# Kernel tuning notes

Measured on AMD Instinct MI355X. Metric: run time of the kernel, lower is better.

The kernel has to match this reference:

```python
import jax, jax.numpy as jnp
import numpy as np

D_MODEL = 1024
D_INNER = 2048   # expand * d_model
D_STATE = 16
D_CONV = 4
DT_RANK = 64     # ceil(d_model / 16)
BATCH = 4
SEQLEN = 2048


def _dw_causal_conv(x, w, b):
    # x: (B, d, L); w: (d, 1, K) depthwise; causal left pad K-1 -> output length L
    y = jax.lax.conv_general_dilated(
        x, w, window_strides=(1,), padding=[(D_CONV - 1, 0)],
        dimension_numbers=("NCH", "OIH", "NCH"), feature_group_count=x.shape[1])
    return y + b[None, :, None]


def _ssm_pass(x_conv, z, A_log, x_proj_w, dt_proj_w, dt_proj_b, D):
    # x_conv, z: (B, d, L)
    Bsz, d, L = x_conv.shape
    u = jax.nn.silu(x_conv)                                   # (B, d, L)
    x_dbl = jnp.einsum("bdl,rd->blr", u, x_proj_w)            # (B, L, dt_rank+2N)
    dt = x_dbl[..., :DT_RANK]
    Bm = x_dbl[..., DT_RANK:DT_RANK + D_STATE]                # (B, L, N)
    Cm = x_dbl[..., DT_RANK + D_STATE:]                       # (B, L, N)
    delta = jax.nn.softplus(jnp.einsum("blr,dr->bld", dt, dt_proj_w) + dt_proj_b)  # (B, L, d)
    A = -jnp.exp(A_log)                                       # (d, N)

    # time-major inputs for scan
    delta_t = jnp.transpose(delta, (1, 0, 2))                 # (L, B, d)
    u_t = jnp.transpose(u, (2, 0, 1))                         # (L, B, d)
    Bm_t = jnp.transpose(Bm, (1, 0, 2))                       # (L, B, N)
    Cm_t = jnp.transpose(Cm, (1, 0, 2))                       # (L, B, N)

    def step(h, inp):
        d_s, B_s, C_s, u_s = inp                              # (B,d) (B,N) (B,N) (B,d)
        dA = jnp.exp(d_s[:, :, None] * A)                     # (B, d, N)
        h = dA * h + (d_s * u_s)[:, :, None] * B_s[:, None, :]
        y = jnp.einsum("bdn,bn->bd", h, C_s)
        return h, y

    h0 = jnp.zeros((Bsz, d, D_STATE), dtype=u.dtype)
    _, ys = jax.lax.scan(step, h0, (delta_t, Bm_t, Cm_t, u_t))  # ys: (L, B, d)
    y = jnp.transpose(ys, (1, 2, 0)) + D[None, :, None] * u     # (B, d, L)
    return y * jax.nn.silu(z)


def setup_inputs() -> dict:
    key = jax.random.key(0)
    ks = jax.random.split(key, 16)
    s = 0.02
    hidden_states = jax.random.normal(ks[0], (BATCH, SEQLEN, D_MODEL), jnp.float32)
    in_proj_w = jax.random.normal(ks[1], (2 * D_INNER, D_MODEL), jnp.float32) * s
    conv_w_f = jax.random.normal(ks[2], (D_INNER, 1, D_CONV), jnp.float32) * 0.2
    conv_b_f = jax.random.normal(ks[3], (D_INNER,), jnp.float32) * 0.1
    conv_w_b = jax.random.normal(ks[4], (D_INNER, 1, D_CONV), jnp.float32) * 0.2
    conv_b_b = jax.random.normal(ks[5], (D_INNER,), jnp.float32) * 0.1
    x_proj_w_f = jax.random.normal(ks[6], (DT_RANK + 2 * D_STATE, D_INNER), jnp.float32) * s
    dt_proj_w_f = jax.random.uniform(ks[7], (D_INNER, DT_RANK), jnp.float32, -DT_RANK**-0.5, DT_RANK**-0.5)
    x_proj_w_b = jax.random.normal(ks[8], (DT_RANK + 2 * D_STATE, D_INNER), jnp.float32) * s
    dt_proj_w_b = jax.random.uniform(ks[9], (D_INNER, DT_RANK), jnp.float32, -DT_RANK**-0.5, DT_RANK**-0.5)
    # dt bias init: inverse-softplus of dt sampled log-uniform in [1e-3, 1e-1]
    dt = jnp.exp(jax.random.uniform(ks[10], (D_INNER,)) * (np.log(0.1) - np.log(0.001)) + np.log(0.001))
    dt = jnp.clip(dt, 1e-4, None)
    inv_dt = dt + jnp.log(-jnp.expm1(-dt))
    dt_proj_b_f = inv_dt
    dt_proj_b_b = inv_dt
    A_log = jnp.log(jnp.broadcast_to(jnp.arange(1, D_STATE + 1, dtype=jnp.float32), (D_INNER, D_STATE)))
    out_proj_w = jax.random.normal(ks[11], (D_MODEL, D_INNER), jnp.float32) * s
    return {
        "hidden_states": hidden_states, "in_proj_w": in_proj_w,
        "conv_w_f": conv_w_f, "conv_b_f": conv_b_f, "conv_w_b": conv_w_b, "conv_b_b": conv_b_b,
        "x_proj_w_f": x_proj_w_f, "dt_proj_w_f": dt_proj_w_f, "dt_proj_b_f": dt_proj_b_f,
        "x_proj_w_b": x_proj_w_b, "dt_proj_w_b": dt_proj_w_b, "dt_proj_b_b": dt_proj_b_b,
        "A_log_f": A_log, "A_log_b": A_log,
        "D_f": jnp.ones((D_INNER,), jnp.float32), "D_b": jnp.ones((D_INNER,), jnp.float32),
        "out_proj_w": out_proj_w,
    }


def reference(hidden_states, in_proj_w, conv_w_f, conv_b_f, conv_w_b, conv_b_b,
              x_proj_w_f, dt_proj_w_f, dt_proj_b_f, x_proj_w_b, dt_proj_w_b, dt_proj_b_b,
              A_log_f, A_log_b, D_f, D_b, out_proj_w):
    L = hidden_states.shape[1]
    xz = jnp.einsum("bld,ed->bel", hidden_states, in_proj_w)  # (B, 2*d_inner, L)
    x, z = xz[:, :D_INNER], xz[:, D_INNER:]

    # forward direction
    x_conv_f = _dw_causal_conv(x, conv_w_f, conv_b_f)[..., :L]
    y_f = _ssm_pass(x_conv_f, z, A_log_f, x_proj_w_f, dt_proj_w_f, dt_proj_b_f, D_f)

    # backward direction
    x_b, z_b = x[..., ::-1], z[..., ::-1]
    x_conv_b = _dw_causal_conv(x_b, conv_w_b, conv_b_b)[..., :L]
    y_b = _ssm_pass(x_conv_b, z_b, A_log_b, x_proj_w_b, dt_proj_w_b, dt_proj_b_b, D_b)[..., ::-1]

    y = (y_f + y_b) / 2.0                                     # if_divide_out=True
    out = jnp.einsum("bdl,ed->ble", y, out_proj_w)            # (B, L, d_model)
    return out
```

## Files before the change

kernel.cpp:

```cpp
#include <hip/hip_runtime.h>


#define Bsz  4
#define LSEQ 2048
#define DM   1024
#define DI   2048
#define DS   16
#define MROWS (Bsz * LSEQ)
#define NCH  32
#define CLEN 64

typedef unsigned short u16b;
typedef __attribute__((ext_vector_type(8))) short short8;
typedef __attribute__((ext_vector_type(4))) float f32x4;
typedef __attribute__((address_space(3))) unsigned int lds_u32;
typedef const __attribute__((address_space(1))) unsigned int glb_u32;

__device__ __forceinline__ float b2f(u16b u) {
  union { unsigned int i; float f; } x; x.i = ((unsigned int)u) << 16; return x.f;
}
__device__ __forceinline__ u16b f2b(float f) {
  union { float f; unsigned int i; } x; x.f = f;
  unsigned int r = x.i + 0x7FFFu + ((x.i >> 16) & 1u);
  return (u16b)(r >> 16);
}
__device__ __forceinline__ u16b f2b_cvt(float f) {
  unsigned int r;
  asm("v_cvt_pk_bf16_f32 %0, %1, %1" : "=v"(r) : "v"(f));
  return (u16b)r;
}
__device__ __forceinline__ float fast_rcp(float x) {
  return __builtin_amdgcn_rcpf(x);
}
__device__ __forceinline__ float softplus_fast(float v) {
  float e = __expf(-fabsf(v));
  return fmaxf(v, 0.f) + __logf(1.f + e);
}
__device__ __forceinline__ void pow_ladder(float q, float* dA) {
  float q2 = q * q, q3 = q2 * q, q4 = q2 * q2;
  float q5 = q4 * q, q6 = q4 * q2, q7 = q4 * q3, q8 = q4 * q4;
  dA[0] = q;  dA[1] = q2;  dA[2] = q3;  dA[3] = q4;
  dA[4] = q5; dA[5] = q6;  dA[6] = q7;  dA[7] = q8;
  dA[8] = q8 * q;  dA[9] = q8 * q2;  dA[10] = q8 * q3;  dA[11] = q8 * q4;
  dA[12] = q8 * q5; dA[13] = q8 * q6; dA[14] = q8 * q7; dA[15] = q8 * q8;
}

__device__ __forceinline__ int xcd_swz(int id, int nwg) {
  int c = nwg >> 3;
  return (id & 7) * c + (id >> 3);
}

__device__ __forceinline__ void stage_tile(const u16b* gbase, int ld,
                                           u16b* lds, int wave, int lane) {
#pragma unroll
  for (int t = 0; t < 4; ++t) {
    int rb = wave * 32 + t * 8;
    int r = rb + (lane >> 3);
    int cb = (lane & 7) ^ (r & 7);
    const u16b* g = gbase + (size_t)r * ld + cb * 8;
    __builtin_amdgcn_global_load_lds((glb_u32*)g, (lds_u32*)(lds + rb * 64),
                                     16, 0, 0);
  }
}

__global__ void sniff_kernel(const unsigned int* __restrict__ p,
                             int* __restrict__ flag) {
  unsigned int w = p[threadIdx.x];
  int e = (w >> 7) & 0xFF;
  unsigned long long m = __ballot(e >= 110 && e <= 135);
  if (threadIdx.x == 0) *flag = (__popcll(m) >= 32) ? 1 : 0;
}

__global__ __launch_bounds__(256) void convert_kernel(
    const void* __restrict__ src, u16b* __restrict__ dst, int n,
    const int* __restrict__ flag) {
  int i = (blockIdx.x * 256 + threadIdx.x) * 8;
  if (i >= n) return;
  if (*flag) {
    *(uint4*)(dst + i) = *(const uint4*)((const u16b*)src + i);
  } else {
    const float* s = (const float*)src;
    float4 a = *(const float4*)(s + i);
    float4 b = *(const float4*)(s + i + 4);
    u16b o[8] = {f2b(a.x), f2b(a.y), f2b(a.z), f2b(a.w),
                 f2b(b.x), f2b(b.y), f2b(b.z), f2b(b.w)};
    *(uint4*)(dst + i) = *(uint4*)o;
  }
}

struct SmallTab { const void* s[14]; u16b* d[14]; };
__global__ __launch_bounds__(256) void convert_small_kernel(
    SmallTab t, const int* __restrict__ flag) {
  const int pref[15] = {0,4,5,9,10,106,170,171,267,331,332,348,364,365,366};
  int bx = blockIdx.x;
  int seg = 0;
#pragma unroll
  for (int i = 0; i < 14; ++i)
    if (bx >= pref[i + 1]) seg = i + 1;
  int idx = (bx - pref[seg]) * 2048 + threadIdx.x * 8;
  u16b* dst = t.d[seg];
  if (*flag) {
    *(uint4*)(dst + idx) = *(const uint4*)((const u16b*)t.s[seg] + idx);
  } else {
    const float* s = (const float*)t.s[seg];
    float4 a = *(const float4*)(s + idx);
    float4 b = *(const float4*)(s + idx + 4);
    u16b o[8] = {f2b(a.x), f2b(a.y), f2b(a.z), f2b(a.w),
                 f2b(b.x), f2b(b.y), f2b(b.z), f2b(b.w)};
    *(uint4*)(dst + idx) = *(uint4*)o;
  }
}

#define BM 128
#define BN 128
#define BK 64

template<int EPI>
__global__ __launch_bounds__(256) void gemm_kernel(
    const u16b* __restrict__ A, const u16b* __restrict__ B, void* __restrict__ Cptr,
    const int* __restrict__ flag, int M, int N, int K, int lda, int ldb, int ldc) {
  __shared__ u16b As[BM * BK];
  __shared__ u16b Bs[BN * BK];
  const int tid = threadIdx.x;
  const int nbx = gridDim.x;
  const int id = xcd_swz(blockIdx.y * nbx + blockIdx.x, nbx * gridDim.y);
  const int n0 = (id % nbx) * BN;
  const int m0 = (id / nbx) * BM;
  const int wave = tid >> 6, lane = tid & 63;
  const int wm = (wave >> 1) * 64, wn = (wave & 1) * 64;
  const int lr = lane & 15, lg = lane >> 4;
  u16b* C = (u16b*)Cptr;
  float* Cf = (float*)Cptr;
  const int fl = (EPI == 3) ? flag[0] : 1;

  f32x4 acc[4][4] = {};

  for (int k0 = 0; k0 < K; k0 += BK) {
    stage_tile(A + (size_t)m0 * lda + k0, lda, As, wave, lane);
    stage_tile(B + (size_t)n0 * ldb + k0, ldb, Bs, wave, lane);
    __syncthreads();
#pragma unroll
    for (int kk = 0; kk < BK; kk += 32) {
      short8 afr[4], bfr[4];
#pragma unroll
      for (int i = 0; i < 4; ++i) {
        int r = wm + i * 16 + lr;
        afr[i] = *(const short8*)&As[r * 64 + (((kk >> 3) + lg) ^ (r & 7)) * 8];
      }
#pragma unroll
      for (int j = 0; j < 4; ++j) {
        int r = wn + j * 16 + lr;
        bfr[j] = *(const short8*)&Bs[r * 64 + (((kk >> 3) + lg) ^ (r & 7)) * 8];
      }
#pragma unroll
      for (int i = 0; i < 4; ++i)
#pragma unroll
        for (int j = 0; j < 4; ++j)
          acc[i][j] = __builtin_amdgcn_mfma_f32_16x16x32_bf16(
              afr[i], bfr[j], acc[i][j], 0, 0, 0);
    }
    __syncthreads();
  }

#pragma unroll
  for (int i = 0; i < 4; ++i) {
    int rbase = m0 + wm + i * 16 + lg * 4;
#pragma unroll
    for (int j = 0; j < 4; ++j) {
      int col = n0 + wn + j * 16 + lr;
      if (col < N) {
#pragma unroll
        for (int e = 0; e < 4; ++e) {
          float v = acc[i][j][e];
          size_t ci = (size_t)(rbase + e) * ldc + col;
          if (EPI == 3) {
            if (fl) C[ci] = f2b(v); else Cf[ci] = v;
          } else {
            C[ci] = f2b(v);
          }
        }
      }
    }
  }
}

template<int EPI>
__global__ __launch_bounds__(256) void gemm2_kernel(
    const u16b* __restrict__ A, const u16b* __restrict__ B1,
    const u16b* __restrict__ B2, u16b* __restrict__ C1, u16b* __restrict__ C2,
    const u16b* __restrict__ bias1, const u16b* __restrict__ bias2,
    float* __restrict__ aux1, float* __restrict__ aux2,
    int Mhalf, int N, int K, int lda, int ldb, int ldc1, int ldc2) {
  __shared__ u16b As[BM * BK];
  __shared__ u16b Bs[BN * BK];
  const int tid = threadIdx.x;
  const int nbx = gridDim.x;
  const int id = xcd_swz(blockIdx.y * nbx + blockIdx.x, nbx * gridDim.y);
  const int n0 = (id % nbx) * BN;
  const int m0 = (id / nbx) * BM;
  const int hi = (m0 >= Mhalf);
  const u16b* B = hi ? B2 : B1;
  u16b* C = hi ? C2 : C1;
  const u16b* bias = hi ? bias2 : bias1;
  float* aux = hi ? aux2 : aux1;
  const int ldc = hi ? ldc2 : ldc1;
  const int mloc = m0 - (hi ? Mhalf : 0);
  const int wave = tid >> 6, lane = tid & 63;
  const int wm = (wave >> 1) * 64, wn = (wave & 1) * 64;
  const int lr = lane & 15, lg = lane >> 4;

  f32x4 acc[4][4] = {};

  for (int k0 = 0; k0 < K; k0 += BK) {
    stage_tile(A + (size_t)m0 * lda + k0, lda, As, wave, lane);
    stage_tile(B + (size_t)n0 * ldb + k0, ldb, Bs, wave, lane);
    __syncthreads();
#pragma unroll
    for (int kk = 0; kk < BK; kk += 32) {
      short8 afr[4], bfr[4];
#pragma unroll
      for (int i = 0; i < 4; ++i) {
        int r = wm + i * 16 + lr;
        afr[i] = *(const short8*)&As[r * 64 + (((kk >> 3) + lg) ^ (r & 7)) * 8];
      }
#pragma unroll
      for (int j = 0; j < 4; ++j) {
        int r = wn + j * 16 + lr;
        bfr[j] = *(const short8*)&Bs[r * 64 + (((kk >> 3) + lg) ^ (r & 7)) * 8];
      }
#pragma unroll
      for (int i = 0; i < 4; ++i)
#pragma unroll
        for (int j = 0; j < 4; ++j)
          acc[i][j] = __builtin_amdgcn_mfma_f32_16x16x32_bf16(
              afr[i], bfr[j], acc[i][j], 0, 0, 0);
    }
    __syncthreads();
  }

#pragma unroll
  for (int i = 0; i < 4; ++i) {
    int rbase = mloc + wm + i * 16 + lg * 4;
#pragma unroll
    for (int j = 0; j < 4; ++j) {
      int col = n0 + wn + j * 16 + lr;
      if (col < N) {
        float bv = (EPI == 1) ? b2f(bias[col]) : 0.f;
#pragma unroll
        for (int e = 0; e < 4; ++e) {
          float v = acc[i][j][e];
          if (EPI == 1) v = softplus_fast(v + bv);
          C[(size_t)(rbase + e) * ldc + col] = f2b(v);
          if (EPI == 2 && col >= 64)
            aux[(size_t)(rbase + e) * 32 + (col - 64)] = v;
        }
      }
    }
  }
}

__global__ __launch_bounds__(256) void gemm2s_kernel(
    const u16b* __restrict__ A, const u16b* __restrict__ B1,
    const u16b* __restrict__ B2, float* __restrict__ P,
    int Mhalf, int Ksplit, int lda, int ldb) {
  __shared__ u16b As[BM * BK];
  __shared__ u16b Bs[BN * BK];
  const int tid = threadIdx.x;
  const int ks = blockIdx.x;
  const int m0 = blockIdx.y * BM;
  const int hi = (m0 >= Mhalf);
  const u16b* B = hi ? B2 : B1;
  const int wave = tid >> 6, lane = tid & 63;
  const int wm = (wave >> 1) * 64, wn = (wave & 1) * 64;
  const int lr = lane & 15, lg = lane >> 4;

  f32x4 acc[4][4] = {};

  const int kbeg = ks * Ksplit;
  for (int k0 = kbeg; k0 < kbeg + Ksplit; k0 += BK) {
    stage_tile(A + (size_t)m0 * lda + k0, lda, As, wave, lane);
    stage_tile(B + k0, ldb, Bs, wave, lane);
    __syncthreads();
#pragma unroll
    for (int kk = 0; kk < BK; kk += 32) {
      short8 afr[4], bfr[4];
#pragma unroll
      for (int i = 0; i < 4; ++i) {
        int r = wm + i * 16 + lr;
        afr[i] = *(const short8*)&As[r * 64 + (((kk >> 3) + lg) ^ (r & 7)) * 8];
      }
#pragma unroll
      for (int j = 0; j < 4; ++j) {
        int r = wn + j * 16 + lr;
        bfr[j] = *(const short8*)&Bs[r * 64 + (((kk >> 3) + lg) ^ (r & 7)) * 8];
      }
#pragma unroll
      for (int i = 0; i < 4; ++i)
#pragma unroll
        for (int j = 0; j < 4; ++j)
          acc[i][j] = __builtin_amdgcn_mfma_f32_16x16x32_bf16(
              afr[i], bfr[j], acc[i][j], 0, 0, 0);
    }
    __syncthreads();
  }

  float* Pk = P + (size_t)ks * ((size_t)2 * Mhalf) * 128;
#pragma unroll
  for (int i = 0; i < 4; ++i) {
    int rg = m0 + wm + i * 16 + lg * 4;
#pragma unroll
    for (int j = 0; j < 4; ++j) {
      int col = wn + j * 16 + lr;
#pragma unroll
      for (int e = 0; e < 4; ++e)
        Pk[(size_t)(rg + e) * 128 + col] = acc[i][j][e];
    }
  }
}

__global__ __launch_bounds__(256) void xdbl_reduce_kernel(
    const float* __restrict__ P, u16b* __restrict__ xdf,
    u16b* __restrict__ xdb, float* __restrict__ bcf,
    float* __restrict__ bcb) {
  int e = blockIdx.x * 256 + threadIdx.x;
  int col = e & 127;
  int m = e >> 7;
  if (col >= 96) return;
  float v = P[(size_t)e] + P[(size_t)e + (size_t)16384 * 128];
  int hi = (m >= MROWS);
  int mloc = m - (hi ? MROWS : 0);
  u16b* C = hi ? xdb : xdf;
  C[(size_t)mloc * 96 + col] = f2b(v);
  if (col >= 64) {
    float* aux = hi ? bcb : bcf;
    aux[(size_t)mloc * 32 + (col - 64)] = v;
  }
}

__global__ __launch_bounds__(256) void conv_kernel(
    const u16b* __restrict__ xz, const u16b* __restrict__ cwf,
    const u16b* __restrict__ cbf, const u16b* __restrict__ cwb,
    const u16b* __restrict__ cbb, u16b* __restrict__ u_f,
    u16b* __restrict__ u_b) {
  int gid = blockIdx.x * 256 + threadIdx.x;
  int d = gid & (DI - 1);
  int m = gid >> 11;
  int b = m >> 11;
  int l = m & (LSEQ - 1);
  const u16b* xcol = xz + ((size_t)b * LSEQ) * (2 * DI) + d;
  float xv[7];
#pragma unroll
  for (int t = 0; t < 7; ++t) {
    int ll = l + t - 3;
    xv[t] = (ll >= 0 && ll < LSEQ) ? b2f(xcol[(size_t)ll * (2 * DI)]) : 0.f;
  }
  float af = b2f(cbf[d]);
#pragma unroll
  for (int k = 0; k < 4; ++k) af = fmaf(b2f(cwf[d * 4 + k]), xv[k], af);
  float ab = b2f(cbb[d]);
#pragma unroll
  for (int j = 0; j < 4; ++j) ab = fmaf(b2f(cwb[d * 4 + 3 - j]), xv[3 + j], ab);
  float sf = af * fast_rcp(1.f + __expf(-af));
  float sb = ab * fast_rcp(1.f + __expf(-ab));
  u_f[(size_t)m * DI + d] = f2b(sf);
  u_b[((size_t)b * LSEQ + (LSEQ - 1 - l)) * DI + d] = f2b(sb);
}

__device__ __forceinline__ bool detect_intA(const u16b* alog, int d, float* An2) {
  bool fast = true;
#pragma unroll
  for (int n = 0; n < DS; ++n) {
    float a = __expf(b2f(alog[d * DS + n]));
    An2[n] = -a * 1.44269504088896f;
    fast = fast && (fabsf(a - (float)(n + 1)) < 0.02f * (float)(n + 1));
  }
  return fast;
}

#define CHUNK_BODY_FAST() do {                                        \
    float du = cd * cu; s += cd;                                      \
    float dA[DS]; pow_ladder(__expf(-cd), dA);                        \
    _Pragma("unroll") for (int n = 0; n < DS; ++n)                    \
      h[n] = fmaf(dA[n], h[n], du * bl[n]);                           \
    bl += 32;                                                         \
  } while (0)

#define CHUNK_BODY_SLOW() do {                                        \
    float du = cd * cu; s += cd;                                      \
    _Pragma("unroll") for (int n = 0; n < DS; ++n) {                  \
      float dA = exp2f(cd * An2[n]);                                  \
      h[n] = fmaf(dA, h[n], du * bl[n]);                              \
    }                                                                 \
    bl += 32;                                                         \
  } while (0)

__global__ __launch_bounds__(256) void scan_chunk_kernel(
    const u16b* __restrict__ xz, const u16b* __restrict__ u_f,
    const u16b* __restrict__ u_b, const u16b* __restrict__ dltb,
    const float* __restrict__ bc_f, const float* __restrict__ bc_b,
    const u16b* __restrict__ alog_f, const u16b* __restrict__ alog_b,
    float* __restrict__ hstate, float* __restrict__ sdelta) {
  int bx = blockIdx.x;
  int dblk = bx & 7;
  int chunk = (bx >> 3) & 31;
  int b = (bx >> 8) & 3;
  int dir = bx >> 10;
  int d = dblk * 256 + threadIdx.x;

  const u16b* uptr = dir ? u_b : u_f;
  const u16b* dlt = dir ? dltb : xz;
  const int ldd = dir ? DI : 2 * DI;
  const float* bcp = dir ? bc_b : bc_f;
  const u16b* alog = dir ? alog_b : alog_f;

  const size_t mb = (size_t)b * LSEQ + (size_t)chunk * CLEN;
  const float* bl = bcp + mb * 32;
  float An2[DS];
  bool fastA = detect_intA(alog, d, An2);

  float h[DS];
#pragma unroll
  for (int n = 0; n < DS; ++n) h[n] = 0.f;
  float s = 0.f;
  unsigned od = (unsigned)mb * (unsigned)ldd + (unsigned)d;
  unsigned ou = (unsigned)mb * DI + (unsigned)d;
  float nd = b2f(dlt[od]);
  float nu = b2f(uptr[ou]);
  float cd, cu;
  if (fastA) {
#pragma unroll 4
    for (int l = 0; l < CLEN - 1; ++l) {
      cd = nd; cu = nu;
      od += ldd; ou += DI;
      nd = b2f(dlt[od]); nu = b2f(uptr[ou]);
      CHUNK_BODY_FAST();
    }
    cd = nd; cu = nu;
    CHUNK_BODY_FAST();
  } else {
#pragma unroll 4
    for (int l = 0; l < CLEN - 1; ++l) {
      cd = nd; cu = nu;
      od += ldd; ou += DI;
      nd = b2f(dlt[od]); nu = b2f(uptr[ou]);
      CHUNK_BODY_SLOW();
    }
    cd = nd; cu = nu;
    CHUNK_BODY_SLOW();
  }
  size_t slot = (size_t)((dir * 4 + b) * 32 + chunk) * 2048 + d;
  float* hp = hstate + slot * 16;
#pragma unroll
  for (int i = 0; i < 4; ++i)
    ((f32x4*)hp)[i] = *(f32x4*)&h[i * 4];
  sdelta[slot] = s;
}

__global__ __launch_bounds__(256) void scan_carry_kernel(
    const u16b* __restrict__ alog_f, const u16b* __restrict__ alog_b,
    float* __restrict__ hstate, const float* __restrict__ sdelta) {
  int gid = blockIdx.x * 256 + threadIdx.x;
  int n = gid & (DS - 1);
  int d = (gid >> 4) & (DI - 1);
  int b = (gid >> 15) & 3;
  int dir = gid >> 17;
  const u16b* alog = dir ? alog_b : alog_f;
  float An2 = -__expf(b2f(alog[d * DS + n])) * 1.44269504088896f;
  float h = 0.f;
  size_t base = (size_t)((dir * 4 + b) * 32) * 2048 + d;
  for (int c = 0; c < NCH; ++c) {
    size_t slot = base + (size_t)c * 2048;
    float sdv = sdelta[slot];
    float* hp = hstate + slot * 16 + n;
    float hl = *hp;
    float P = exp2f(An2 * sdv);
    float nh = fmaf(P, h, hl);
    *hp = h;
    h = nh;
  }
}

#define APPLY_BODY_FAST() do {                                        \
    float du = cd * cu;                                               \
    float dA[DS]; pow_ladder(__expf(-cd), dA);                        \
    float y0 = 0.f, y1 = 0.f;                                         \
    _Pragma("unroll") for (int n = 0; n < DS; n += 2) {               \
      h[n] = fmaf(dA[n], h[n], du * bl[n]);                           \
      y0 = fmaf(h[n], bl[16 + n], y0);                                \
      h[n + 1] = fmaf(dA[n + 1], h[n + 1], du * bl[n + 1]);           \
      y1 = fmaf(h[n + 1], bl[17 + n], y1);                            \
    }                                                                 \
    float sz = cz * fast_rcp(1.f + __expf(-cz));                      \
    float out = (y0 + y1 + Dd * cu) * sz;                             \
    uptr[oo] = f2b_cvt(out); oo += DI; bl += 32;                      \
  } while (0)

#define APPLY_BODY_SLOW() do {                                        \
    float du = cd * cu;                                               \
    float y = 0.f;                                                    \
    _Pragma("unroll") for (int n = 0; n < DS; ++n) {                  \
      float dA = exp2f(cd * An2[n]);                                  \
      h[n] = fmaf(dA, h[n], du * bl[n]);                              \
      y = fmaf(h[n], bl[16 + n], y);                                  \
    }                                                                 \
    float sz = cz * fast_rcp(1.f + __expf(-cz));                      \
    float out = (y + Dd * cu) * sz;                                   \
    uptr[oo] = f2b_cvt(out); oo += DI; bl += 32;                      \
  } while (0)

__global__ __launch_bounds__(256) void scan_apply_kernel(
    const u16b* __restrict__ xz, u16b* __restrict__ u_f,
    u16b* __restrict__ u_b, const u16b* __restrict__ dltb,
    const float* __restrict__ bc_f, const float* __restrict__ bc_b,
    const u16b* __restrict__ alog_f, const u16b* __restrict__ alog_b,
    const u16b* __restrict__ dv_f, const u16b* __restrict__ dv_b,
    const float* __restrict__ hstate) {
  int bx = blockIdx.x;
  int dblk = bx & 7;
  int chunk = (bx >> 3) & 31;
  int b = (bx >> 8) & 3;
  int dir = bx >> 10;
  int d = dblk * 256 + threadIdx.x;

  u16b* uptr = dir ? u_b : u_f;
  const u16b* dlt = dir ? dltb : xz;
  const int ldd = dir ? DI : 2 * DI;
  const float* bcp = dir ? bc_b : bc_f;
  const u16b* alog = dir ? alog_b : alog_f;
  const u16b* dv = dir ? dv_b : dv_f;

  const size_t mb0 = (size_t)b * LSEQ;
  const size_t mb = mb0 + (size_t)chunk * CLEN;
  const float* bl = bcp + mb * 32;
  float An2[DS];
  bool fastA = detect_intA(alog, d, An2);
  float Dd = b2f(dv[d]);
  float h[DS];
  {
    size_t slot = (size_t)((dir * 4 + b) * 32 + chunk) * 2048 + d;
    const float* hp = hstate + slot * 16;
#pragma unroll
    for (int i = 0; i < 4; ++i)
      *(f32x4*)&h[i * 4] = ((const f32x4*)hp)[i];
  }

  size_t zs0 = dir ? (mb0 + (LSEQ - 1 - (size_t)chunk * CLEN)) : mb;
  const int zst = dir ? -(2 * DI) : (2 * DI);
  unsigned od = (unsigned)mb * (unsigned)ldd + (unsigned)d;
  unsigned ou = (unsigned)mb * DI + (unsigned)d;
  unsigned oo = ou;
  int oz = (int)zs0 * (2 * DI) + DI + d;
  float nd = b2f(dlt[od]);
  float nu = b2f(uptr[ou]);
  float nz = b2f(xz[oz]);
  float cd, cu, cz;
  if (fastA) {
#pragma unroll 4
    for (int l = 0; l < CLEN - 1; ++l) {
      cd = nd; cu = nu; cz = nz;
      od += ldd; ou += DI; oz += zst;
      nd = b2f(dlt[od]); nu = b2f(uptr[ou]); nz = b2f(xz[oz]);
      APPLY_BODY_FAST();
    }
    cd = nd; cu = nu; cz = nz;
    APPLY_BODY_FAST();
  } else {
#pragma unroll 4
    for (int l = 0; l < CLEN - 1; ++l) {
      cd = nd; cu = nu; cz = nz;
      od += ldd; ou += DI; oz += zst;
      nd = b2f(dlt[od]); nu = b2f(uptr[ou]); nz = b2f(xz[oz]);
      APPLY_BODY_SLOW();
    }
    cd = nd; cu = nu; cz = nz;
    APPLY_BODY_SLOW();
  }
}

__global__ __launch_bounds__(256) void combine_kernel(
    const u16b* __restrict__ yf, const u16b* __restrict__ yb_rev,
    u16b* __restrict__ yc) {
  size_t i = ((size_t)blockIdx.x * 256 + threadIdx.x) * 8;
  size_t m = i >> 11;
  size_t dcol = i & (DI - 1);
  size_t mr = m ^ (LSEQ - 1);
  uint4 a = *(const uint4*)(yf + m * DI + dcol);
  uint4 b = *(const uint4*)(yb_rev + mr * DI + dcol);
  const u16b* ap = (const u16b*)&a;
  const u16b* bp = (const u16b*)&b;
  uint4 o;
  u16b* op = (u16b*)&o;
#pragma unroll
  for (int j = 0; j < 8; ++j) op[j] = f2b(0.5f * (b2f(ap[j]) + b2f(bp[j])));
  *(uint4*)(yc + i) = o;
}

extern "C" void kernel_launch(void* const* d_in, const int* in_sizes, int n_in,
                              void* d_out, int out_size, void* d_ws,
                              size_t ws_size, hipStream_t stream) {
  char* ws = (char*)d_ws;
  u16b* xz    = (u16b*)(ws);
  u16b* u_f   = (u16b*)(ws + 67108864);
  u16b* u_b   = (u16b*)(ws + 100663296);
  u16b* arena = (u16b*)(ws + 134217728);
  u16b* xdf   = (u16b*)(ws + 167772160);
  u16b* xdb   = (u16b*)(ws + 169345024);
  float* bcf  = (float*)(ws + 170917888);
  float* bcb  = (float*)(ws + 171966464);
  u16b* opw_c  = (u16b*)(ws + 173015040);
  u16b* xpwf_c = (u16b*)(ws + 177209344);
  u16b* xpwb_c = (u16b*)(ws + 177602560);
  u16b* dpwf_c = (u16b*)(ws + 177995776);
  u16b* dpwb_c = (u16b*)(ws + 178257920);
  u16b* cwf_c  = (u16b*)(ws + 178520064);
  u16b* cwb_c  = (u16b*)(ws + 178536448);
  u16b* cbf_c  = (u16b*)(ws + 178552832);
  u16b* cbb_c  = (u16b*)(ws + 178556928);
  u16b* dpbf_c = (u16b*)(ws + 178561024);
  u16b* dpbb_c = (u16b*)(ws + 178565120);
  u16b* alf_c  = (u16b*)(ws + 178569216);
  u16b* alb_c  = (u16b*)(ws + 178634752);
  u16b* dvf_c  = (u16b*)(ws + 178700288);
  u16b* dvb_c  = (u16b*)(ws + 178704384);
  int*  flag   = (int*)(ws + 178708480);
  float* hstate = (float*)(ws + 178712576);
  float* sdelta = (float*)(ws + 212267008);

  u16b* hs_c  = arena;
  u16b* inw_c = arena + 8388608;
  float* Pbuf = (float*)arena;
  u16b* dltb  = arena;
  u16b* y_c   = arena;

  dim3 blk(256);
  sniff_kernel<<<dim3(1), dim3(64), 0, stream>>>((const unsigned int*)d_in[0], flag);
  convert_kernel<<<dim3(4096), blk, 0, stream>>>(d_in[0], hs_c, 8388608, flag);
  convert_kernel<<<dim3(2048), blk, 0, stream>>>(d_in[1], inw_c, 4194304, flag);
  convert_kernel<<<dim3(1024), blk, 0, stream>>>(d_in[16], opw_c, 2097152, flag);
  SmallTab st = {{d_in[2], d_in[3], d_in[4], d_in[5], d_in[6], d_in[7], d_in[8],
                  d_in[9], d_in[10], d_in[11], d_in[12], d_in[13], d_in[14],
                  d_in[15]},
                 {cwf_c, cbf_c, cwb_c, cbb_c, xpwf_c, dpwf_c, dpbf_c, xpwb_c,
                  dpwb_c, dpbb_c, alf_c, alb_c, dvf_c, dvb_c}};
  convert_small_kernel<<<dim3(366), blk, 0, stream>>>(st, flag);

  gemm_kernel<0><<<dim3(32, 64), blk, 0, stream>>>(hs_c, inw_c, xz, flag,
      MROWS, 2 * DI, DM, DM, DM, 2 * DI);
  conv_kernel<<<dim3(65536), blk, 0, stream>>>(xz, cwf_c, cbf_c, cwb_c, cbb_c,
                                               u_f, u_b);
  gemm2s_kernel<<<dim3(2, 128), blk, 0, stream>>>(u_f, xpwf_c, xpwb_c, Pbuf,
      MROWS, 1024, DI, DI);
  xdbl_reduce_kernel<<<dim3(8192), blk, 0, stream>>>(Pbuf, xdf, xdb, bcf, bcb);
  gemm2_kernel<1><<<dim3(16, 128), blk, 0, stream>>>(xdf, dpwf_c, dpwb_c,
      xz, dltb, dpbf_c, dpbb_c, nullptr, nullptr, MROWS, DI, 64, 96, 64,
      2 * DI, DI);
  scan_chunk_kernel<<<dim3(2048), blk, 0, stream>>>(xz, u_f, u_b, dltb, bcf,
      bcb, alf_c, alb_c, hstate, sdelta);
  scan_carry_kernel<<<dim3(1024), blk, 0, stream>>>(alf_c, alb_c, hstate, sdelta);
  scan_apply_kernel<<<dim3(2048), blk, 0, stream>>>(xz, u_f, u_b, dltb, bcf,
      bcb, alf_c, alb_c, dvf_c, dvb_c, hstate);
  combine_kernel<<<dim3(8192), blk, 0, stream>>>(u_f, u_b, y_c);
  gemm_kernel<3><<<dim3(8, 64), blk, 0, stream>>>(y_c, opw_c, d_out, flag,
      MROWS, DM, DI, DI, DI, DM);
}
```

Baseline: 550.3 us.

## Use 256x256 double-buffered 8-wave GEMM for input projection

Replaces the 128x128 single-stage GEMM for the in_proj matmul with a new 512-thread kernel using 256x256 tiles, double-buffered LDS and global loads interleaved across four compute sub-phases. The larger tile raises arithmetic intensity per LDS byte and the prefetch overlaps global loads with MFMA work. In exchange it uses 128KB of LDS per block, which limits occupancy, and the grid has only 512 blocks, so wave quantization and barrier overhead become a risk. The original epilogue template (EPI=0) is bypassed; the new kernel writes bf16 directly.

```diff
diff --git a/kernel.cpp b/kernel.cpp
--- a/kernel.cpp
+++ b/kernel.cpp
@@ -60,6 +60,19 @@
     const u16b* g = gbase + (size_t)r * ld + cb * 8;
     __builtin_amdgcn_global_load_lds((glb_u32*)g, (lds_u32*)(lds + rb * 64),
                                      16, 0, 0);
+  }
+}
+
+__device__ __forceinline__ void stage_half(const u16b* gbase, int ld,
+                                           u16b* ldsbase, int tid) {
+#pragma unroll
+  for (int i2 = 0; i2 < 2; ++i2) {
+    int rg = (tid >> 6) * 2 + i2;
+    int row = rg * 8 + ((tid >> 3) & 7);
+    int cb = (tid & 7) ^ (row & 7);
+    const u16b* g = gbase + (size_t)row * ld + cb * 8;
+    __builtin_amdgcn_global_load_lds((glb_u32*)g,
+                                     (lds_u32*)(ldsbase + rg * 8 * 64), 16, 0, 0);
   }
 }
 
@@ -108,6 +121,101 @@
     u16b o[8] = {f2b(a.x), f2b(a.y), f2b(a.z), f2b(a.w),
                  f2b(b.x), f2b(b.y), f2b(b.z), f2b(b.w)};
     *(uint4*)(dst + idx) = *(uint4*)o;
+  }
+}
+
+__global__ __launch_bounds__(512, 2) void gemm8_kernel(
+    const u16b* __restrict__ A, const u16b* __restrict__ B,
+    u16b* __restrict__ C, int M, int N, int K, int lda, int ldb, int ldc) {
+  __shared__ u16b As[2][256 * 64];
+  __shared__ u16b Bs[2][256 * 64];
+  const int tid = threadIdx.x;
+  const int nbx = gridDim.x;
+  const int id = xcd_swz(blockIdx.y * nbx + blockIdx.x, nbx * gridDim.y);
+  const int n0 = (id % nbx) * 256;
+  const int m0 = (id / nbx) * 256;
+  const int wave = tid >> 6, lane = tid & 63;
+  const int wm = (wave >> 2) * 128, wn = (wave & 3) * 64;
+  const int lr = lane & 15, lg = lane >> 4;
+
+  const u16b* Ab = A + (size_t)m0 * lda;
+  const u16b* Bb = B + (size_t)n0 * ldb;
+  const int nt = K >> 6;
+
+  f32x4 acc[8][4] = {};
+
+  stage_half(Ab, lda, As[0], tid);
+  stage_half(Ab + (size_t)128 * lda, lda, As[0] + 8192, tid);
+  stage_half(Bb, ldb, Bs[0], tid);
+  stage_half(Bb + (size_t)128 * ldb, ldb, Bs[0] + 8192, tid);
+  asm volatile("s_waitcnt vmcnt(0)" ::: "memory");
+  __builtin_amdgcn_s_barrier();
+
+  for (int t = 0; t < nt; ++t) {
+    const int cur = t & 1;
+    const u16b* Ac = As[cur];
+    const u16b* Bc = Bs[cur];
+    u16b* An = As[cur ^ 1];
+    u16b* Bn = Bs[cur ^ 1];
+    const int k1 = (t + 1) << 6;
+    const bool more = (t + 1 < nt);
+#pragma unroll
+    for (int q = 0; q < 4; ++q) {
+      short8 afr[4][2], bfr[2][2];
+#pragma unroll
+      for (int i = 0; i < 4; ++i) {
+        int r = wm + (q >> 1) * 64 + i * 16 + lr;
+#pragma unroll
+        for (int kx = 0; kx < 2; ++kx)
+          afr[i][kx] = *(const short8*)&Ac[r * 64 + ((kx * 4 + lg) ^ (r & 7)) * 8];
+      }
+#pragma unroll
+      for (int j = 0; j < 2; ++j) {
+        int r = wn + (q & 1) * 32 + j * 16 + lr;
+#pragma unroll
+        for (int kx = 0; kx < 2; ++kx)
+          bfr[j][kx] = *(const short8*)&Bc[r * 64 + ((kx * 4 + lg) ^ (r & 7)) * 8];
+      }
+      if (more) {
+        if (q == 0) stage_half(Ab + k1, lda, An, tid);
+        else if (q == 1) stage_half(Ab + (size_t)128 * lda + k1, lda, An + 8192, tid);
+        else if (q == 2) stage_half(Bb + k1, ldb, Bn, tid);
+        else stage_half(Bb + (size_t)128 * ldb + k1, ldb, Bn + 8192, tid);
+      }
+      __builtin_amdgcn_s_barrier();
+      asm volatile("s_waitcnt lgkmcnt(0)" ::: "memory");
+      __builtin_amdgcn_sched_barrier(0);
+      __builtin_amdgcn_s_setprio(1);
+#pragma unroll
+      for (int kx = 0; kx < 2; ++kx)
+#pragma unroll
+        for (int i = 0; i < 4; ++i)
+#pragma unroll
+          for (int j = 0; j < 2; ++j)
+            acc[(q >> 1) * 4 + i][(q & 1) * 2 + j] =
+                __builtin_amdgcn_mfma_f32_16x16x32_bf16(
+                    afr[i][kx], bfr[j][kx],
+                    acc[(q >> 1) * 4 + i][(q & 1) * 2 + j], 0, 0, 0);
+      __builtin_amdgcn_s_setprio(0);
+      __builtin_amdgcn_sched_barrier(0);
+      __builtin_amdgcn_s_barrier();
+    }
+    asm volatile("s_waitcnt vmcnt(0)" ::: "memory");
+    __builtin_amdgcn_s_barrier();
+  }
+
+#pragma unroll
+  for (int i = 0; i < 8; ++i) {
+    int rbase = m0 + wm + i * 16 + lg * 4;
+#pragma unroll
+    for (int j = 0; j < 4; ++j) {
+      int col = n0 + wn + j * 16 + lr;
+      if (col < N) {
+#pragma unroll
+        for (int e = 0; e < 4; ++e)
+          C[(size_t)(rbase + e) * ldc + col] = f2b(acc[i][j][e]);
+      }
+    }
   }
 }
 
@@ -644,7 +752,7 @@
                   dpwb_c, dpbb_c, alf_c, alb_c, dvf_c, dvb_c}};
   convert_small_kernel<<<dim3(366), blk, 0, stream>>>(st, flag);
 
-  gemm_kernel<0><<<dim3(32, 64), blk, 0, stream>>>(hs_c, inw_c, xz, flag,
+  gemm8_kernel<<<dim3(16, 32), dim3(512), 0, stream>>>(hs_c, inw_c, xz,
       MROWS, 2 * DI, DM, DM, DM, 2 * DI);
   conv_kernel<<<dim3(65536), blk, 0, stream>>>(xz, cwf_c, cbf_c, cwb_c, cbb_c,
                                                u_f, u_b);
```

Result: no change. 548.1 us (-0.4%).
